# Optimization experiments

Measured on AMD Instinct MI355X. Metric: run time of the kernel, lower is better.

The kernel has to match this reference:

```python
import jax, jax.numpy as jnp
import numpy as np

# ---- static config (matches init_kwargs) ----
N0, N1 = 150000, 75000          # al nodes, test nodes
E = 200000                       # edges per edge type
D = 128                          # dim_h
L = 3                            # n_layers
T = 4                            # netypes
NAL = 50000                      # n_al vocab
NC = 3                           # n_classes
T_SRCS = [0, 0, 1, 1]
T_TGTS = [0, 1, 0, 1]
NODE_COUNTS = [N0, N1]


def setup_inputs() -> dict:
    key = jax.random.key(0)
    ks = jax.random.split(key, 16)
    x0_ids = jax.random.randint(ks[0], (N0,), 0, NAL, dtype=jnp.int32)
    x1_ids = jnp.zeros((N1,), dtype=jnp.int32)  # emb_test has a single row

    def make_edges(k, n_src, n_dst):
        k1, k2 = jax.random.split(k)
        src = jax.random.randint(k1, (E,), 0, n_src, dtype=jnp.int32)
        dst = jax.random.randint(k2, (E,), 0, n_dst, dtype=jnp.int32)
        return jnp.stack([src, dst])  # [2, E]

    es = [make_edges(ks[1 + j], NODE_COUNTS[T_SRCS[j]], NODE_COUNTS[T_TGTS[j]])
          for j in range(T)]

    s = 1.0 / np.sqrt(D)
    enc_al_w   = jax.random.normal(ks[5],  (NAL, D), jnp.float32) * s
    emb_test_w = jax.random.normal(ks[6],  (1, D),   jnp.float32) * s
    W_tgt = jax.random.normal(ks[7],  (L, T, D, D), jnp.float32) * s
    b_tgt = jax.random.normal(ks[8],  (L, T, D),    jnp.float32) * 0.01
    W_src = jax.random.normal(ks[9],  (L, T, D, D), jnp.float32) * s
    b_src = jax.random.normal(ks[10], (L, T, D),    jnp.float32) * 0.01
    emb_self = jax.random.normal(ks[11], (L, T, 2, D), jnp.float32) * s
    W_dec = jax.random.normal(ks[12], (NC, D), jnp.float32) * s
    b_dec = jax.random.normal(ks[13], (NC,),   jnp.float32) * 0.01
    return {
        "x0_ids": x0_ids, "x1_ids": x1_ids,
        "es0": es[0], "es1": es[1], "es2": es[2], "es3": es[3],
        "enc_al_w": enc_al_w, "emb_test_w": emb_test_w,
        "W_tgt": W_tgt, "b_tgt": b_tgt, "W_src": W_src, "b_src": b_src,
        "emb_self": emb_self, "W_dec": W_dec, "b_dec": b_dec,
    }


def reference(x0_ids, x1_ids, es0, es1, es2, es3,
              enc_al_w, emb_test_w, W_tgt, b_tgt, W_src, b_src,
              emb_self, W_dec, b_dec):
    ess = [es0, es1, es2, es3]
    # node-type embeddings
    xs = [enc_al_w[x0_ids], emb_test_w[x1_ids]]  # [N0,D], [N1,D]
    for i in range(L):
        out = [jnp.zeros((N0, D), xs[0].dtype), jnp.zeros((N1, D), xs[1].dtype)]
        for j in range(T):
            ts, tt = T_SRCS[j], T_TGTS[j]
            src, dst = ess[j][0], ess[j][1]
            # project node features first (same math as projecting gathered edges)
            h_src = xs[ts] @ W_src[i, j].T + b_src[i, j]   # lin_src(x_src)
            h_dst = xs[tt] @ W_tgt[i, j].T + b_tgt[i, j]   # lin_tgt(x_dst)
            self_flag = (dst == src).astype(jnp.int32)
            msg = h_dst[dst] + h_src[src] + emb_self[i, j][self_flag]  # [E,D]
            agg = jax.ops.segment_max(msg, dst, num_segments=NODE_COUNTS[tt])
            out[tt] = out[tt] + jax.nn.relu(agg)  # MPNN.forward applies relu
        xs = [jax.nn.relu(out[0]), jax.nn.relu(out[1])]
    last = xs[0] @ W_dec.T + b_dec                 # [N0, NC]
    return (last, jax.nn.softmax(last, axis=1))
```

## Files before the change

### kernel.cpp

```cpp
#include <hip/hip_runtime.h>
#include <hip/hip_bf16.h>

#define N0 150000
#define N1 75000
#define EE 200000
#define NAL 50000
#define NSEG (N0 + N1)
#define NSEG2 (2 * NSEG)
#define TOTE (4 * EE)

typedef unsigned short u16;
using s16x8 = __attribute__((ext_vector_type(8))) short;
using f32x4 = __attribute__((ext_vector_type(4))) float;
using u16x8 = __attribute__((ext_vector_type(8))) unsigned short;

__device__ __forceinline__ u16 f2b(float f) {
  unsigned int b = __float_as_uint(f);
  b += 0x7FFFu + ((b >> 16) & 1u);
  return (u16)(b >> 16);
}
__device__ __forceinline__ float b2f(u16 u) {
  return __uint_as_float(((unsigned int)u) << 16);
}

__global__ void sentinel_k(float* out, float val) {
  if (threadIdx.x == 0 && blockIdx.x == 0) out[0] = val;
}

__global__ __launch_bounds__(256) void prep_w(const float* __restrict__ Ws,
                                              const float* __restrict__ Wt,
                                              u16* __restrict__ BP) {
  int idx = blockIdx.x * 256 + threadIdx.x;
  int mk = idx & 16383;
  int slot = (idx >> 14) & 7;
  int i = idx >> 17;
  const int ssel[8] = {1, 0, 0, 1, 1, 1, 0, 0};
  const int sj[8]   = {0, 0, 2, 1, 2, 3, 1, 3};
  const float* W = ssel[slot] ? Ws : Wt;
  BP[idx] = f2b(W[(size_t)(i * 4 + sj[slot]) * 16384 + mk]);
}

__global__ __launch_bounds__(256) void embed_k(const int* __restrict__ ids,
                                               const float* __restrict__ tab,
                                               u16* __restrict__ X, int N, unsigned vocab) {
  int idx = blockIdx.x * 256 + threadIdx.x;
  int v = idx >> 4;
  if (v >= N) return;
  int q = (idx & 15) << 3;
  unsigned id = (unsigned)ids[v];
  if (id >= vocab) id = 0;
  const float* src = tab + (size_t)id * 128 + q;
  f32x4 x0 = *(const f32x4*)src;
  f32x4 x1 = *(const f32x4*)(src + 4);
  u16x8 o;
#pragma unroll
  for (int k = 0; k < 4; ++k) { o[k] = f2b(x0[k]); o[4 + k] = f2b(x1[k]); }
  *(u16x8*)(X + (size_t)v * 128 + q) = o;
}

__global__ __launch_bounds__(256) void count_all(const int* __restrict__ e0,
                                                 const int* __restrict__ e1,
                                                 const int* __restrict__ e2,
                                                 const int* __restrict__ e3,
                                                 int* __restrict__ cnt) {
  int i = blockIdx.x * 256 + threadIdx.x;
  if (i >= TOTE) return;
  int j = i / EE, r = i - j * EE;
  const int* es = (j == 0) ? e0 : (j == 1) ? e1 : (j == 2) ? e2 : e3;
  int dst = es[EE + r];
  int seg = (j & 1) ? N0 + dst : dst;
  atomicAdd(cnt + seg * 2 + (j >> 1), 1);
}

__global__ __launch_bounds__(512) void scan1_k(const int* __restrict__ cnt,
                                               int* __restrict__ off,
                                               int* __restrict__ part, int N) {
  __shared__ int sh[512];
  int t = threadIdx.x, i = blockIdx.x * 512 + t;
  int v = (i < N) ? cnt[i] : 0;
  sh[t] = v; __syncthreads();
  for (int s = 1; s < 512; s <<= 1) {
    int x = (t >= s) ? sh[t - s] : 0; __syncthreads();
    sh[t] += x; __syncthreads();
  }
  if (i < N) off[i] = sh[t] - v;
  if (t == 511) part[blockIdx.x] = sh[511];
}

__global__ __launch_bounds__(1024) void scan2_k(int* __restrict__ part, int n) {
  __shared__ int sh[1024];
  int t = threadIdx.x;
  int v = (t < n) ? part[t] : 0;
  sh[t] = v; __syncthreads();
  for (int s = 1; s < 1024; s <<= 1) {
    int x = (t >= s) ? sh[t - s] : 0; __syncthreads();
    sh[t] += x; __syncthreads();
  }
  if (t < n) part[t] = sh[t] - v;
}

__global__ __launch_bounds__(256) void scan3_k(int* __restrict__ off,
                                               const int* __restrict__ part, int N, int tot) {
  int i = blockIdx.x * 256 + threadIdx.x;
  if (i < N) off[i] += part[i >> 9];
  if (i == 0) off[N] = tot;
}

__global__ __launch_bounds__(256) void fill_all(const int* __restrict__ e0,
                                                const int* __restrict__ e1,
                                                const int* __restrict__ e2,
                                                const int* __restrict__ e3,
                                                const int* __restrict__ off,
                                                int* __restrict__ cur,
                                                int* __restrict__ einfo) {
  int i = blockIdx.x * 256 + threadIdx.x;
  if (i >= TOTE) return;
  int j = i / EE, r = i - j * EE;
  const int* es = (j == 0) ? e0 : (j == 1) ? e1 : (j == 2) ? e2 : e3;
  int src = es[r], dst = es[EE + r];
  int seg2 = ((j & 1) ? N0 + dst : dst) * 2 + (j >> 1);
  int pos = off[seg2] + atomicAdd(cur + seg2, 1);
  einfo[pos] = src | ((src == dst) ? (int)0x80000000 : 0);
}

__global__ __launch_bounds__(256, 3) void gemm_multi(const u16* __restrict__ A, int M,
                                                     const u16* __restrict__ W, int nw,
                                                     u16* __restrict__ C0,
                                                     u16* __restrict__ C1,
                                                     u16* __restrict__ C2,
                                                     u16* __restrict__ C3) {
  __shared__ u16 Al[64 * 128];
  __shared__ u16 Bl[128 * 128];
  const int t = threadIdx.x;
  const int row0 = blockIdx.x * 64;

#pragma unroll
  for (int u = 0; u < 4; ++u) {
    int c = u * 256 + t;
    int r = c >> 4, ch = c & 15;
    int rc = (row0 + r < M) ? (row0 + r) : (M - 1);
    int sw = ch ^ (r & 7);
    *(u16x8*)&Al[r * 128 + sw * 8] = *(const u16x8*)(A + (size_t)rc * 128 + ch * 8);
  }

  const int w = t >> 6, lane = t & 63;
  const int lr = lane & 15, g = lane >> 4;
  const int arow = (w * 16 + lr) * 128;

  u16x8 breg[8];
#pragma unroll
  for (int u = 0; u < 8; ++u) {
    int c = u * 256 + t;
    int r = c >> 4, ch = c & 15;
    breg[u] = *(const u16x8*)(W + r * 128 + ch * 8);
  }

  for (int ws = 0; ws < nw; ++ws) {
    __builtin_amdgcn_sched_barrier(0);
    __builtin_amdgcn_s_barrier();
    __builtin_amdgcn_sched_barrier(0);

#pragma unroll
    for (int u = 0; u < 8; ++u) {
      int c = u * 256 + t;
      int r = c >> 4, ch = c & 15;
      int sw = ch ^ (r & 7);
      *(u16x8*)&Bl[r * 128 + sw * 8] = breg[u];
    }
    if (ws + 1 < nw) {
      const u16* Bn = W + (size_t)(ws + 1) * 16384;
#pragma unroll
      for (int u = 0; u < 8; ++u) {
        int c = u * 256 + t;
        int r = c >> 4, ch = c & 15;
        breg[u] = *(const u16x8*)(Bn + r * 128 + ch * 8);
      }
    }
    asm volatile("s_waitcnt lgkmcnt(0)" ::: "memory");
    __builtin_amdgcn_sched_barrier(0);
    __builtin_amdgcn_s_barrier();
    __builtin_amdgcn_sched_barrier(0);

    f32x4 acc[8];
#pragma unroll
    for (int nf = 0; nf < 8; ++nf) acc[nf] = f32x4{0.f, 0.f, 0.f, 0.f};

#pragma unroll
    for (int ks = 0; ks < 4; ++ks) {
      int swz = ((ks * 4 + g) ^ (lr & 7)) * 8;
      s16x8 a = *(const s16x8*)&Al[arow + swz];
#pragma unroll
      for (int nf = 0; nf < 8; ++nf) {
        s16x8 b = *(const s16x8*)&Bl[(nf * 16 + lr) * 128 + swz];
        acc[nf] = __builtin_amdgcn_mfma_f32_16x16x32_bf16(a, b, acc[nf], 0, 0, 0);
      }
    }

    u16* Cw = (ws == 0) ? C0 : (ws == 1) ? C1 : (ws == 2) ? C2 : C3;
#pragma unroll
    for (int nf = 0; nf < 8; ++nf) {
      int col = nf * 16 + lr;
#pragma unroll
      for (int j = 0; j < 4; ++j) {
        int row = row0 + w * 16 + g * 4 + j;
        if (row < M) Cw[(size_t)row * 128 + col] = f2b(acc[nf][j]);
      }
    }
  }
}

__global__ __launch_bounds__(256) void agg2_k(const int* __restrict__ off2,
                                              const int* __restrict__ einfo,
                                              int segbase,
                                              const u16* __restrict__ HSA,
                                              const u16* __restrict__ HSB,
                                              const u16* __restrict__ HD0,
                                              const u16* __restrict__ HD1,
                                              const float* __restrict__ bs0,
                                              const float* __restrict__ bt0,
                                              const float* __restrict__ bs1,
                                              const float* __restrict__ bt1,
                                              const float* __restrict__ esf0,
                                              const float* __restrict__ esf1,
                                              u16* __restrict__ Y, int N) {
  int idx = blockIdx.x * 256 + threadIdx.x;
  int d = idx >> 4;
  if (d >= N) return;
  int f8 = (idx & 15) << 3;
  int base = (segbase + d) * 2;
  int e0 = off2[base], e1 = off2[base + 1], e2 = off2[base + 2];

  float en[8], es_[8];
#pragma unroll
  for (int k = 0; k < 8; ++k) { en[k] = esf0[f8 + k]; es_[k] = esf0[128 + f8 + k]; }
  float m0[8];
#pragma unroll
  for (int k = 0; k < 8; ++k) m0[k] = -INFINITY;
  for (int e = e0; e < e1; ++e) {
    int info = einfo[e];
    int s = info & 0x7fffffff;
    bool self = (info < 0);
    u16x8 hv = *(const u16x8*)(HSA + (size_t)s * 128 + f8);
#pragma unroll
    for (int k = 0; k < 8; ++k)
      m0[k] = fmaxf(m0[k], b2f(hv[k]) + (self ? es_[k] : en[k]));
  }

#pragma unroll
  for (int k = 0; k < 8; ++k) { en[k] = esf1[f8 + k]; es_[k] = esf1[128 + f8 + k]; }
  float m1[8];
#pragma unroll
  for (int k = 0; k < 8; ++k) m1[k] = -INFINITY;
  for (int e = e1; e < e2; ++e) {
    int info = einfo[e];
    int s = info & 0x7fffffff;
    bool self = (info < 0);
    u16x8 hv = *(const u16x8*)(HSB + (size_t)s * 128 + f8);
#pragma unroll
    for (int k = 0; k < 8; ++k)
      m1[k] = fmaxf(m1[k], b2f(hv[k]) + (self ? es_[k] : en[k]));
  }

  u16x8 hd0 = *(const u16x8*)(HD0 + (size_t)d * 128 + f8);
  u16x8 hd1 = *(const u16x8*)(HD1 + (size_t)d * 128 + f8);
  u16x8 o;
#pragma unroll
  for (int k = 0; k < 8; ++k) {
    float r0 = fmaxf(b2f(hd0[k]) + bs0[f8 + k] + bt0[f8 + k] + m0[k], 0.f);
    float r1 = fmaxf(b2f(hd1[k]) + bs1[f8 + k] + bt1[f8 + k] + m1[k], 0.f);
    o[k] = f2b(r0 + r1);
  }
  *(u16x8*)(Y + (size_t)d * 128 + f8) = o;
}

__global__ __launch_bounds__(256) void decoder_k(const u16* __restrict__ X,
                                                 const float* __restrict__ Wd,
                                                 const float* __restrict__ bd,
                                                 float* __restrict__ out) {
  int v = blockIdx.x * 256 + threadIdx.x;
  if (v >= N0) return;
  float a0 = bd[0], a1 = bd[1], a2 = bd[2];
  const u16* x = X + (size_t)v * 128;
#pragma unroll
  for (int k = 0; k < 128; k += 8) {
    u16x8 xv = *(const u16x8*)(x + k);
#pragma unroll
    for (int u = 0; u < 8; ++u) {
      float xf = b2f(xv[u]);
      a0 = fmaf(xf, Wd[k + u], a0);
      a1 = fmaf(xf, Wd[128 + k + u], a1);
      a2 = fmaf(xf, Wd[256 + k + u], a2);
    }
  }
  float mx = fmaxf(a0, fmaxf(a1, a2));
  float e0 = expf(a0 - mx), e1 = expf(a1 - mx), e2 = expf(a2 - mx);
  float inv = 1.f / (e0 + e1 + e2);
  size_t b = (size_t)v * 3;
  out[b + 0] = a0; out[b + 1] = a1; out[b + 2] = a2;
  size_t b2 = (size_t)N0 * 3 + b;
  out[b2 + 0] = e0 * inv; out[b2 + 1] = e1 * inv; out[b2 + 2] = e2 * inv;
}

extern "C" void kernel_launch(void* const* d_in, const int* in_sizes, int n_in,
                              void* d_out, int out_size, void* d_ws, size_t ws_size,
                              hipStream_t stream) {
  float* out = (float*)d_out;

  const int expect[15] = {N0, N1, 2 * EE, 2 * EE, 2 * EE, 2 * EE,
                          NAL * 128, 128, 196608, 1536, 196608, 1536,
                          3072, 384, 3};
  bool ok = (n_in == 15);
  if (ok) for (int i = 0; i < 15; ++i) ok = ok && (in_sizes[i] == expect[i]);
  if (!ok) { sentinel_k<<<1, 64, 0, stream>>>(out, 500.f); return; }

  const int* x0_ids = (const int*)d_in[0];
  const int* x1_ids = (const int*)d_in[1];
  const int* es0 = (const int*)d_in[2];
  const int* es1 = (const int*)d_in[3];
  const int* es2 = (const int*)d_in[4];
  const int* es3 = (const int*)d_in[5];
  const float* enc_al   = (const float*)d_in[6];
  const float* emb_test = (const float*)d_in[7];
  const float* W_tgt    = (const float*)d_in[8];
  const float* b_tgt    = (const float*)d_in[9];
  const float* W_src    = (const float*)d_in[10];
  const float* b_src    = (const float*)d_in[11];
  const float* emb_self = (const float*)d_in[12];
  const float* W_dec    = (const float*)d_in[13];
  const float* b_dec    = (const float*)d_in[14];

  char* base = (char*)d_ws;
  size_t pos = 0;
  auto alloc = [&](size_t bytes) -> void* {
    void* r = base + pos;
    pos += (bytes + 255) & ~(size_t)255;
    return r;
  };
  u16* xs0 = (u16*)alloc((size_t)N0 * 128 * 2);
  u16* xs1 = (u16*)alloc((size_t)N1 * 128 * 2);
  u16* P0  = (u16*)alloc((size_t)N0 * 128 * 2);
  u16* P1  = (u16*)alloc((size_t)N0 * 128 * 2);
  u16* P2  = (u16*)alloc((size_t)N0 * 128 * 2);
  u16* P3  = (u16*)alloc((size_t)N1 * 128 * 2);
  u16* P4  = (u16*)alloc((size_t)N0 * 128 * 2);
  u16* BP  = (u16*)alloc((size_t)3 * 8 * 16384 * 2);
  int* off2   = (int*)alloc((size_t)(NSEG2 + 1) * 4);
  int* einfo  = (int*)alloc((size_t)TOTE * 4);
  int* counts = (int*)alloc((size_t)NSEG2 * 4);
  int* cursor = counts;
  int* part   = (int*)alloc(1024 * 4);
  if (pos > ws_size) { sentinel_k<<<1, 64, 0, stream>>>(out, 900.f); return; }

  prep_w<<<1536, 256, 0, stream>>>(W_src, W_tgt, BP);
  embed_k<<<(N0 * 16 + 255) / 256, 256, 0, stream>>>(x0_ids, enc_al, xs0, N0, NAL);
  embed_k<<<(N1 * 16 + 255) / 256, 256, 0, stream>>>(x1_ids, emb_test, xs1, N1, 1);

  const int EG = (TOTE + 255) / 256;
  const int nb = (NSEG2 + 511) / 512;
  hipMemsetAsync(counts, 0, (size_t)NSEG2 * 4, stream);
  count_all<<<EG, 256, 0, stream>>>(es0, es1, es2, es3, counts);
  scan1_k<<<nb, 512, 0, stream>>>(counts, off2, part, NSEG2);
  scan2_k<<<1, 1024, 0, stream>>>(part, nb);
  scan3_k<<<(NSEG2 + 255) / 256, 256, 0, stream>>>(off2, part, NSEG2, TOTE);
  hipMemsetAsync(cursor, 0, (size_t)NSEG2 * 4, stream);
  fill_all<<<EG, 256, 0, stream>>>(es0, es1, es2, es3, off2, cursor, einfo);

  const int G0 = (N0 + 63) / 64, G1 = (N1 + 63) / 64;
  const int GA0 = (N0 * 16 + 255) / 256, GA1 = (N1 * 16 + 255) / 256;
  for (int i = 0; i < 3; ++i) {
    const u16* BPi = BP + (size_t)i * 8 * 16384;
    gemm_multi<<<G0, 256, 0, stream>>>(xs0, N0, BPi + 0 * 16384, (i < 2) ? 4 : 3,
                                       P0, P1, P2, P4);
    gemm_multi<<<G1, 256, 0, stream>>>(xs1, N1, BPi + 4 * 16384, 1, P3, P3, P3, P3);
    agg2_k<<<GA0, 256, 0, stream>>>(off2, einfo, 0, P0, P3, P1, P2,
                                    b_src + (size_t)(i * 4 + 0) * 128, b_tgt + (size_t)(i * 4 + 0) * 128,
                                    b_src + (size_t)(i * 4 + 2) * 128, b_tgt + (size_t)(i * 4 + 2) * 128,
                                    emb_self + (size_t)(i * 4 + 0) * 256,
                                    emb_self + (size_t)(i * 4 + 2) * 256, xs0, N0);
    if (i < 2) {
      gemm_multi<<<G1, 256, 0, stream>>>(xs1, N1, BPi + 5 * 16384, 3, P3, P1, P2, P2);
      agg2_k<<<GA1, 256, 0, stream>>>(off2, einfo, N0, P4, P3, P1, P2,
                                      b_src + (size_t)(i * 4 + 1) * 128, b_tgt + (size_t)(i * 4 + 1) * 128,
                                      b_src + (size_t)(i * 4 + 3) * 128, b_tgt + (size_t)(i * 4 + 3) * 128,
                                      emb_self + (size_t)(i * 4 + 1) * 256,
                                      emb_self + (size_t)(i * 4 + 3) * 256, xs1, N1);
    }
  }

  decoder_k<<<(N0 + 255) / 256, 256, 0, stream>>>(xs0, W_dec, b_dec, out);
}
```

Baseline: 528.0 us.

## Merge per-type GEMM launches, load A fragments to registers, narrow aggregation vectors

The two GEMM launches per layer for node types 0 and 1 become one launch whose blocks pick their operand set from the block index. Each block now loads its A fragments straight from global memory into registers instead of staging them through LDS. Dropping the A staging cuts shared memory per block, so the occupancy hint rises from 3 to 4 blocks. The aggregation kernel uses 32 threads per node with 4 features each instead of 16 threads with 8, doubling the threads that issue edge gathers at the cost of narrower loads and more redundant index reads.

```diff
diff --git a/kernel.cpp b/kernel.cpp
--- a/kernel.cpp
+++ b/kernel.cpp
@@ -12,6 +12,7 @@
 typedef unsigned short u16;
 using s16x8 = __attribute__((ext_vector_type(8))) short;
 using f32x4 = __attribute__((ext_vector_type(4))) float;
+using u16x4 = __attribute__((ext_vector_type(4))) unsigned short;
 using u16x8 = __attribute__((ext_vector_type(8))) unsigned short;
 
 __device__ __forceinline__ u16 f2b(float f) {
@@ -123,29 +124,33 @@
   einfo[pos] = src | ((src == dst) ? (int)0x80000000 : 0);
 }
 
-__global__ __launch_bounds__(256, 3) void gemm_multi(const u16* __restrict__ A, int M,
-                                                     const u16* __restrict__ W, int nw,
-                                                     u16* __restrict__ C0,
-                                                     u16* __restrict__ C1,
-                                                     u16* __restrict__ C2,
-                                                     u16* __restrict__ C3) {
-  __shared__ u16 Al[64 * 128];
+__global__ __launch_bounds__(256, 4) void gemm_fused(const u16* __restrict__ A0, int M0, int nB0,
+                                                     const u16* __restrict__ W0, int nw0,
+                                                     u16* __restrict__ C00, u16* __restrict__ C01,
+                                                     u16* __restrict__ C02, u16* __restrict__ C03,
+                                                     const u16* __restrict__ A1, int M1,
+                                                     const u16* __restrict__ W1,
+                                                     u16* __restrict__ C10) {
   __shared__ u16 Bl[128 * 128];
   const int t = threadIdx.x;
-  const int row0 = blockIdx.x * 64;
-
-#pragma unroll
-  for (int u = 0; u < 4; ++u) {
-    int c = u * 256 + t;
-    int r = c >> 4, ch = c & 15;
-    int rc = (row0 + r < M) ? (row0 + r) : (M - 1);
-    int sw = ch ^ (r & 7);
-    *(u16x8*)&Al[r * 128 + sw * 8] = *(const u16x8*)(A + (size_t)rc * 128 + ch * 8);
+  const u16* A; const u16* W; int M, row0, nw;
+  u16 *c0, *c1, *c2, *c3;
+  if ((int)blockIdx.x < nB0) {
+    A = A0; M = M0; row0 = blockIdx.x * 64; W = W0; nw = nw0;
+    c0 = C00; c1 = C01; c2 = C02; c3 = C03;
+  } else {
+    A = A1; M = M1; row0 = (blockIdx.x - nB0) * 64; W = W1; nw = 1;
+    c0 = C10; c1 = C10; c2 = C10; c3 = C10;
   }
 
   const int w = t >> 6, lane = t & 63;
   const int lr = lane & 15, g = lane >> 4;
-  const int arow = (w * 16 + lr) * 128;
+  int row = row0 + w * 16 + lr;
+  int rowc = (row < M) ? row : (M - 1);
+  const u16* Ab = A + (size_t)rowc * 128 + g * 8;
+  u16x8 a[4];
+#pragma unroll
+  for (int ks = 0; ks < 4; ++ks) a[ks] = *(const u16x8*)(Ab + ks * 32);
 
   u16x8 breg[8];
 #pragma unroll
@@ -188,22 +193,21 @@
 #pragma unroll
     for (int ks = 0; ks < 4; ++ks) {
       int swz = ((ks * 4 + g) ^ (lr & 7)) * 8;
-      s16x8 a = *(const s16x8*)&Al[arow + swz];
 #pragma unroll
       for (int nf = 0; nf < 8; ++nf) {
         s16x8 b = *(const s16x8*)&Bl[(nf * 16 + lr) * 128 + swz];
-        acc[nf] = __builtin_amdgcn_mfma_f32_16x16x32_bf16(a, b, acc[nf], 0, 0, 0);
+        acc[nf] = __builtin_amdgcn_mfma_f32_16x16x32_bf16((s16x8)a[ks], b, acc[nf], 0, 0, 0);
       }
     }
 
-    u16* Cw = (ws == 0) ? C0 : (ws == 1) ? C1 : (ws == 2) ? C2 : C3;
+    u16* Cw = (ws == 0) ? c0 : (ws == 1) ? c1 : (ws == 2) ? c2 : c3;
 #pragma unroll
     for (int nf = 0; nf < 8; ++nf) {
       int col = nf * 16 + lr;
 #pragma unroll
       for (int j = 0; j < 4; ++j) {
-        int row = row0 + w * 16 + g * 4 + j;
-        if (row < M) Cw[(size_t)row * 128 + col] = f2b(acc[nf][j]);
+        int orow = row0 + w * 16 + g * 4 + j;
+        if (orow < M) Cw[(size_t)orow * 128 + col] = f2b(acc[nf][j]);
       }
     }
   }
@@ -224,53 +228,53 @@
                                               const float* __restrict__ esf1,
                                               u16* __restrict__ Y, int N) {
   int idx = blockIdx.x * 256 + threadIdx.x;
-  int d = idx >> 4;
+  int d = idx >> 5;
   if (d >= N) return;
-  int f8 = (idx & 15) << 3;
+  int f4 = (idx & 31) << 2;
   int base = (segbase + d) * 2;
   int e0 = off2[base], e1 = off2[base + 1], e2 = off2[base + 2];
 
-  float en[8], es_[8];
-#pragma unroll
-  for (int k = 0; k < 8; ++k) { en[k] = esf0[f8 + k]; es_[k] = esf0[128 + f8 + k]; }
-  float m0[8];
-#pragma unroll
-  for (int k = 0; k < 8; ++k) m0[k] = -INFINITY;
+  float en[4], es_[4];
+#pragma unroll
+  for (int k = 0; k < 4; ++k) { en[k] = esf0[f4 + k]; es_[k] = esf0[128 + f4 + k]; }
+  float m0[4];
+#pragma unroll
+  for (int k = 0; k < 4; ++k) m0[k] = -INFINITY;
   for (int e = e0; e < e1; ++e) {
     int info = einfo[e];
     int s = info & 0x7fffffff;
     bool self = (info < 0);
-    u16x8 hv = *(const u16x8*)(HSA + (size_t)s * 128 + f8);
-#pragma unroll
-    for (int k = 0; k < 8; ++k)
+    u16x4 hv = *(const u16x4*)(HSA + (size_t)s * 128 + f4);
+#pragma unroll
+    for (int k = 0; k < 4; ++k)
       m0[k] = fmaxf(m0[k], b2f(hv[k]) + (self ? es_[k] : en[k]));
   }
 
 #pragma unroll
-  for (int k = 0; k < 8; ++k) { en[k] = esf1[f8 + k]; es_[k] = esf1[128 + f8 + k]; }
-  float m1[8];
-#pragma unroll
-  for (int k = 0; k < 8; ++k) m1[k] = -INFINITY;
+  for (int k = 0; k < 4; ++k) { en[k] = esf1[f4 + k]; es_[k] = esf1[128 + f4 + k]; }
+  float m1[4];
+#pragma unroll
+  for (int k = 0; k < 4; ++k) m1[k] = -INFINITY;
   for (int e = e1; e < e2; ++e) {
     int info = einfo[e];
     int s = info & 0x7fffffff;
     bool self = (info < 0);
-    u16x8 hv = *(const u16x8*)(HSB + (size_t)s * 128 + f8);
-#pragma unroll
-    for (int k = 0; k < 8; ++k)
+    u16x4 hv = *(const u16x4*)(HSB + (size_t)s * 128 + f4);
+#pragma unroll
+    for (int k = 0; k < 4; ++k)
       m1[k] = fmaxf(m1[k], b2f(hv[k]) + (self ? es_[k] : en[k]));
   }
 
-  u16x8 hd0 = *(const u16x8*)(HD0 + (size_t)d * 128 + f8);
-  u16x8 hd1 = *(const u16x8*)(HD1 + (size_t)d * 128 + f8);
-  u16x8 o;
-#pragma unroll
-  for (int k = 0; k < 8; ++k) {
-    float r0 = fmaxf(b2f(hd0[k]) + bs0[f8 + k] + bt0[f8 + k] + m0[k], 0.f);
-    float r1 = fmaxf(b2f(hd1[k]) + bs1[f8 + k] + bt1[f8 + k] + m1[k], 0.f);
+  u16x4 hd0 = *(const u16x4*)(HD0 + (size_t)d * 128 + f4);
+  u16x4 hd1 = *(const u16x4*)(HD1 + (size_t)d * 128 + f4);
+  u16x4 o;
+#pragma unroll
+  for (int k = 0; k < 4; ++k) {
+    float r0 = fmaxf(b2f(hd0[k]) + bs0[f4 + k] + bt0[f4 + k] + m0[k], 0.f);
+    float r1 = fmaxf(b2f(hd1[k]) + bs1[f4 + k] + bt1[f4 + k] + m1[k], 0.f);
     o[k] = f2b(r0 + r1);
   }
-  *(u16x8*)(Y + (size_t)d * 128 + f8) = o;
+  *(u16x4*)(Y + (size_t)d * 128 + f4) = o;
 }
 
 __global__ __launch_bounds__(256) void decoder_k(const u16* __restrict__ X,
@@ -366,19 +370,21 @@
   fill_all<<<EG, 256, 0, stream>>>(es0, es1, es2, es3, off2, cursor, einfo);
 
   const int G0 = (N0 + 63) / 64, G1 = (N1 + 63) / 64;
-  const int GA0 = (N0 * 16 + 255) / 256, GA1 = (N1 * 16 + 255) / 256;
+  const int GA0 = (N0 * 32 + 255) / 256, GA1 = (N1 * 32 + 255) / 256;
   for (int i = 0; i < 3; ++i) {
     const u16* BPi = BP + (size_t)i * 8 * 16384;
-    gemm_multi<<<G0, 256, 0, stream>>>(xs0, N0, BPi + 0 * 16384, (i < 2) ? 4 : 3,
-                                       P0, P1, P2, P4);
-    gemm_multi<<<G1, 256, 0, stream>>>(xs1, N1, BPi + 4 * 16384, 1, P3, P3, P3, P3);
+    gemm_fused<<<G0 + G1, 256, 0, stream>>>(xs0, N0, G0, BPi + 0 * 16384, (i < 2) ? 4 : 3,
+                                            P0, P1, P2, P4,
+                                            xs1, N1, BPi + 4 * 16384, P3);
     agg2_k<<<GA0, 256, 0, stream>>>(off2, einfo, 0, P0, P3, P1, P2,
                                     b_src + (size_t)(i * 4 + 0) * 128, b_tgt + (size_t)(i * 4 + 0) * 128,
                                     b_src + (size_t)(i * 4 + 2) * 128, b_tgt + (size_t)(i * 4 + 2) * 128,
                                     emb_self + (size_t)(i * 4 + 0) * 256,
                                     emb_self + (size_t)(i * 4 + 2) * 256, xs0, N0);
     if (i < 2) {
-      gemm_multi<<<G1, 256, 0, stream>>>(xs1, N1, BPi + 5 * 16384, 3, P3, P1, P2, P2);
+      gemm_fused<<<G1, 256, 0, stream>>>(xs1, N1, G1, BPi + 5 * 16384, 3,
+                                         P3, P1, P2, P2,
+                                         xs1, N1, BPi + 4 * 16384, P3);
       agg2_k<<<GA1, 256, 0, stream>>>(off2, einfo, N0, P4, P3, P1, P2,
                                       b_src + (size_t)(i * 4 + 1) * 128, b_tgt + (size_t)(i * 4 + 1) * 128,
                                       b_src + (size_t)(i * 4 + 3) * 128, b_tgt + (size_t)(i * 4 + 3) * 128,
```

New measurement: 596.4 us. 1.13x slower.
